# Kernel tuning notes

Measured on AMD Instinct MI355X. Metric: run time of the kernel, lower is better.

Reference implementation:

```python
import jax, jax.numpy as jnp
import numpy as np

N_NODES = 10000
N_EDGES = 320000
F = 128
N_RBF = 20


def setup_inputs() -> dict:
    key = jax.random.key(0)
    ks = jax.random.split(key, 12)
    inp = {
        "idx_i": jax.random.randint(ks[0], (N_EDGES,), 0, N_NODES),
        "idx_j": jax.random.randint(ks[1], (N_EDGES,), 0, N_NODES),
        "rel_dir": jax.random.normal(ks[2], (N_EDGES, 3), dtype=jnp.float32),
        "rel_dist_cut": jax.random.uniform(ks[3], (N_EDGES,), dtype=jnp.float32),
        "rbf_features": jax.random.normal(ks[4], (N_EDGES, N_RBF), dtype=jnp.float32),
        "scalar_features": jax.random.normal(ks[5], (N_NODES, F), dtype=jnp.float32),
        "vector_features": jax.random.normal(ks[6], (N_NODES, F, 3), dtype=jnp.float32),
        # learned params: scalar_network = Linear(F,F) -> SiLU -> Linear(F,3F); rbf_network = Linear(N_RBF,3F)
        "W1": jax.random.normal(ks[7], (F, F), dtype=jnp.float32) / np.sqrt(F),
        "b1": jnp.zeros((F,), dtype=jnp.float32),
        "W2": jax.random.normal(ks[8], (F, 3 * F), dtype=jnp.float32) / np.sqrt(F),
        "b2": jnp.zeros((3 * F,), dtype=jnp.float32),
        "Wr": jax.random.normal(ks[9], (N_RBF, 3 * F), dtype=jnp.float32) / np.sqrt(N_RBF),
        "br": jnp.zeros((3 * F,), dtype=jnp.float32),
    }
    return inp


def reference(idx_i, idx_j, rel_dir, rel_dist_cut, rbf_features,
              scalar_features, vector_features, W1, b1, W2, b2, Wr, br):
    num_nodes, num_features = scalar_features.shape
    # per-node MLP: [N, 3F]
    phi = jax.nn.silu(scalar_features @ W1 + b1) @ W2 + b2
    # distance gate: [E, 3F]
    Wg = (rbf_features @ Wr + br) * rel_dist_cut[:, None]
    # gather neighbor phi and gate
    phi_W = phi[idx_j] * Wg                       # [E, 3F]
    phi_W_vv = phi_W[:, :num_features]            # [E, F]
    phi_W_ss = phi_W[:, num_features:2 * num_features]
    phi_W_vs = phi_W[:, 2 * num_features:]
    # per-receiver edge counts (bincount)
    counts = jax.ops.segment_sum(jnp.ones((idx_i.shape[0],), phi_W.dtype),
                                 idx_i, num_segments=num_nodes)  # [N]
    scalar_residuals = jax.ops.segment_sum(phi_W_ss, idx_i, num_segments=num_nodes)
    scalar_residuals = scalar_residuals / counts[:, None]
    # per-edge vector message: [E, F, 3]
    v_edge = (vector_features[idx_j] * phi_W_vv[:, :, None]
              + phi_W_vs[:, :, None] * rel_dir[:, None, :])
    vector_residuals = jax.ops.segment_sum(v_edge, idx_i, num_segments=num_nodes)
    vector_residuals = vector_residuals / counts[:, None, None]
    return (scalar_features + scalar_residuals,
            vector_features + vector_residuals)
```

## Files before the change

kernel.cpp:

```cpp
#include <hip/hip_runtime.h>
#include <hip/hip_bf16.h>

#define NN 10000
#define NE 320000
#define FDIM 128
#define NRBF 20
#define PHI_DIM 384
#define NKEY NN
#define SCAN_BLOCKS 40

typedef unsigned int uint;
typedef unsigned short ushort;

#if __has_builtin(__builtin_amdgcn_fdot2_f32_bf16)
#define USE_DOT2 1
typedef __bf16 bf16x2 __attribute__((ext_vector_type(2)));
#else
#define USE_DOT2 0
#endif

__device__ __forceinline__ ushort f2bf(float x) {
  __hip_bfloat16 b = __float2bfloat16(x);
  return *(ushort*)&b;
}
__device__ __forceinline__ float bflo(uint u) { return __uint_as_float(u << 16); }
__device__ __forceinline__ float bfhi(uint u) { return __uint_as_float(u & 0xffff0000u); }


__global__ __launch_bounds__(256) void phi_kernel(
    const float* __restrict__ S, const float* __restrict__ W1, const float* __restrict__ b1,
    const float* __restrict__ W2, const float* __restrict__ b2, const float* __restrict__ vf,
    const int* __restrict__ idx_i, int* __restrict__ counts, char* __restrict__ tab) {
  __shared__ float s_s[8][FDIM];
  __shared__ float h_s[8][FDIM];
  const int t = threadIdx.x;
  const int tf = t & 127;
  const int half = t >> 7;
  const int nb = blockIdx.x * 8 + half * 4;
  const int row0 = half * 4;
  atomicAdd(&counts[idx_i[blockIdx.x * 256 + t]], 1);
#pragma unroll
  for (int n = 0; n < 4; n++) s_s[row0 + n][tf] = S[(nb + n) * FDIM + tf];
  __syncthreads();
  float acc[4];
#pragma unroll
  for (int n = 0; n < 4; n++) acc[n] = 0.f;
  for (int k = 0; k < FDIM; k++) {
    float w = W1[k * FDIM + tf];
#pragma unroll
    for (int n = 0; n < 4; n++) acc[n] += s_s[row0 + n][k] * w;
  }
  float bb = b1[tf];
#pragma unroll
  for (int n = 0; n < 4; n++) {
    float x = acc[n] + bb;
    h_s[row0 + n][tf] = x / (1.0f + expf(-x));
  }
  __syncthreads();
  float a0[4], a1[4], a2[4];
#pragma unroll
  for (int n = 0; n < 4; n++) { a0[n] = 0.f; a1[n] = 0.f; a2[n] = 0.f; }
  for (int k = 0; k < FDIM; k++) {
    float w0 = W2[k * PHI_DIM + tf];
    float w1 = W2[k * PHI_DIM + tf + 128];
    float w2 = W2[k * PHI_DIM + tf + 256];
#pragma unroll
    for (int n = 0; n < 4; n++) {
      float hv = h_s[row0 + n][k];
      a0[n] += hv * w0;
      a1[n] += hv * w1;
      a2[n] += hv * w2;
    }
  }
  float c0 = b2[tf], c1 = b2[tf + 128], c2 = b2[tf + 256];
#pragma unroll
  for (int n = 0; n < 4; n++) {
    const int node = nb + n;
    const float p0 = a0[n] + c0;
    const float p1 = a1[n] + c1;
    const float p2 = a2[n] + c2;
    const float* src = vf + (size_t)node * (FDIM * 3) + tf * 3;
    const uint wx = f2bf(src[0] * p0);
    const uint wy = f2bf(src[1] * p0);
    const uint wz = f2bf(src[2] * p0);
    char* pb = tab + (size_t)node * 1280;
    ((uint*)pb)[tf] = (wy << 16) | wx;
    ((uint*)(pb + 512))[tf] = ((uint)f2bf(p1) << 16) | wz;
    ((ushort*)(pb + 1024))[tf] = f2bf(p2);
  }
}

__global__ void scan1_kernel(const int* __restrict__ counts, int* __restrict__ offsets,
                             int* __restrict__ blocksums) {
  __shared__ int s[256];
  const int t = threadIdx.x;
  const int idx = blockIdx.x * 256 + t;
  const int c = counts[idx];
  s[t] = c;
  __syncthreads();
  for (int off = 1; off < 256; off <<= 1) {
    int v = (t >= off) ? s[t - off] : 0;
    __syncthreads();
    s[t] += v;
    __syncthreads();
  }
  if (idx < NKEY) offsets[idx] = s[t] - c;
  if (t == 255) blocksums[blockIdx.x] = s[255];
}

__global__ void scan2_kernel(int* __restrict__ blocksums, int* __restrict__ offsets) {
  __shared__ int s[64];
  const int t = threadIdx.x;
  int v0 = (t < SCAN_BLOCKS) ? blocksums[t] : 0;
  s[t] = v0;
  __syncthreads();
  for (int off = 1; off < 64; off <<= 1) {
    int v = (t >= off) ? s[t - off] : 0;
    __syncthreads();
    s[t] += v;
    __syncthreads();
  }
  if (t < SCAN_BLOCKS) blocksums[t] = s[t] - v0;
  if (t == SCAN_BLOCKS - 1) offsets[NKEY] = s[t];
}

__global__ void stage_kernel(const int* __restrict__ idx_i, const int* __restrict__ idx_j,
                             const float* __restrict__ cut, const float* __restrict__ dir,
                             const float* __restrict__ rbf, const int* __restrict__ offsets,
                             const int* __restrict__ blocksums, int* __restrict__ counts,
                             uint* __restrict__ edata, int* __restrict__ jlist) {
  int e = blockIdx.x * blockDim.x + threadIdx.x;
  if (e >= NE) return;
  int i = idx_i[e];
  int pos = atomicSub(&counts[i], 1) - 1;
  const int slot = offsets[i] + blocksums[i >> 8] + pos;
  jlist[slot] = idx_j[e];
  const float c = cut[e];
  uint w[12];
  w[0] = ((uint)f2bf(dir[e * 3 + 1]) << 16) | f2bf(dir[e * 3 + 0]);
  const float* rb = rbf + (size_t)e * NRBF;
#pragma unroll
  for (int r = 0; r < 10; r++) {
    uint lo = (uint)f2bf(rb[2 * r] * c);
    uint hi = (uint)f2bf(rb[2 * r + 1] * c);
    w[1 + r] = (hi << 16) | lo;
  }
  w[11] = ((uint)f2bf(dir[e * 3 + 2]) << 16) | f2bf(c);
  uint4* d = (uint4*)(edata + (size_t)slot * 12);
  d[0] = make_uint4(w[0], w[1], w[2], w[3]);
  d[1] = make_uint4(w[4], w[5], w[6], w[7]);
  d[2] = make_uint4(w[8], w[9], w[10], w[11]);
}

__global__ __launch_bounds__(128, 5) void node_kernel(
    const uint* __restrict__ edata, const int* __restrict__ jlist,
    const float* __restrict__ Wr, const float* __restrict__ br,
    const char* __restrict__ tab, const float* __restrict__ sf,
    const float* __restrict__ vf, const int* __restrict__ offsets,
    const int* __restrict__ blocksums, float* __restrict__ out) {
  const int f = threadIdx.x;
#if USE_DOT2
  bf16x2 wrA[11], wrB[11], wrC[11];
#pragma unroll
  for (int r = 0; r < 10; r++) {
    uint a = ((uint)f2bf(Wr[(2 * r + 1) * PHI_DIM + f]) << 16) | f2bf(Wr[(2 * r) * PHI_DIM + f]);
    uint b = ((uint)f2bf(Wr[(2 * r + 1) * PHI_DIM + f + 128]) << 16) |
             f2bf(Wr[(2 * r) * PHI_DIM + f + 128]);
    uint c = ((uint)f2bf(Wr[(2 * r + 1) * PHI_DIM + f + 256]) << 16) |
             f2bf(Wr[(2 * r) * PHI_DIM + f + 256]);
    wrA[r] = __builtin_bit_cast(bf16x2, a);
    wrB[r] = __builtin_bit_cast(bf16x2, b);
    wrC[r] = __builtin_bit_cast(bf16x2, c);
  }
  wrA[10] = __builtin_bit_cast(bf16x2, (uint)f2bf(br[f]));
  wrB[10] = __builtin_bit_cast(bf16x2, (uint)f2bf(br[f + 128]));
  wrC[10] = __builtin_bit_cast(bf16x2, (uint)f2bf(br[f + 256]));
#else
  float wrA[22], wrB[22], wrC[22];
#pragma unroll
  for (int r = 0; r < NRBF; r++) {
    wrA[r] = Wr[r * PHI_DIM + f];
    wrB[r] = Wr[r * PHI_DIM + f + 128];
    wrC[r] = Wr[r * PHI_DIM + f + 256];
  }
  wrA[20] = br[f];       wrA[21] = 0.f;
  wrB[20] = br[f + 128]; wrB[21] = 0.f;
  wrC[20] = br[f + 256]; wrC[21] = 0.f;
#endif
  const int n = blockIdx.x;
  const int beg = __builtin_amdgcn_readfirstlane(offsets[n] + blocksums[n >> 8]);
  const int end = __builtin_amdgcn_readfirstlane(
      (n + 1 < NKEY) ? (offsets[n + 1] + blocksums[(n + 1) >> 8]) : offsets[NKEY]);
  float ss = 0.f, ax = 0.f, ay = 0.f, az = 0.f;
  const int f4 = f * 4;

  auto process = [&](uint4 e0, uint4 e1, uint4 e2, uint d0, uint d1, uint zu) {
    uint rbp[11] = {e0.y, e0.z, e0.w, e1.x, e1.y, e1.z, e1.w, e2.x, e2.y, e2.z, e2.w};
    const float dx = bflo(e0.x);
    const float dy = bfhi(e0.x);
    const float dz = bfhi(rbp[10]);
    float g0 = 0.f, g1 = 0.f, g2 = 0.f;
#if USE_DOT2
#pragma unroll
    for (int r = 0; r < 11; r++) {
      bf16x2 rp = __builtin_bit_cast(bf16x2, rbp[r]);
      g0 = __builtin_amdgcn_fdot2_f32_bf16(rp, wrA[r], g0, false);
      g1 = __builtin_amdgcn_fdot2_f32_bf16(rp, wrB[r], g1, false);
      g2 = __builtin_amdgcn_fdot2_f32_bf16(rp, wrC[r], g2, false);
    }
#else
#pragma unroll
    for (int r = 0; r < 11; r++) {
      float rlo = bflo(rbp[r]);
      float rhi = bfhi(rbp[r]);
      g0 += rlo * wrA[2 * r] + rhi * wrA[2 * r + 1];
      g1 += rlo * wrB[2 * r] + rhi * wrB[2 * r + 1];
      g2 += rlo * wrC[2 * r] + rhi * wrC[2 * r + 1];
    }
#endif
    const float vs = bflo(zu) * g2;
    ss += bfhi(d1) * g1;
    ax += bflo(d0) * g0 + vs * dx;
    ay += bfhi(d0) * g0 + vs * dy;
    az += bflo(d1) * g0 + vs * dz;
  };

  int p = beg;
  for (; p + 2 <= end; p += 2) {
    const int j0 = __builtin_amdgcn_readfirstlane(jlist[p]);
    const int j1 = __builtin_amdgcn_readfirstlane(jlist[p + 1]);
    const char* B0 = tab + (size_t)j0 * 1280;
    const char* B1 = tab + (size_t)j1 * 1280;
    const uint d00 = *(const uint*)(B0 + f4), d01 = *(const uint*)(B0 + 512 + f4);
    const uint z0 = *(const ushort*)(B0 + 1024 + f * 2);
    const uint d10 = *(const uint*)(B1 + f4), d11 = *(const uint*)(B1 + 512 + f4);
    const uint z1 = *(const ushort*)(B1 + 1024 + f * 2);
    const uint4* r0 = (const uint4*)(edata + (size_t)p * 12);
    const uint4* r1 = (const uint4*)(edata + (size_t)(p + 1) * 12);
    uint4 a0 = r0[0], a1 = r0[1], a2 = r0[2];
    uint4 b0 = r1[0], b1 = r1[1], b2 = r1[2];
    process(a0, a1, a2, d00, d01, z0);
    process(b0, b1, b2, d10, d11, z1);
  }
  if (p < end) {
    const int j0 = __builtin_amdgcn_readfirstlane(jlist[p]);
    const char* B0 = tab + (size_t)j0 * 1280;
    const uint d00 = *(const uint*)(B0 + f4), d01 = *(const uint*)(B0 + 512 + f4);
    const uint z0 = *(const ushort*)(B0 + 1024 + f * 2);
    const uint4* r0 = (const uint4*)(edata + (size_t)p * 12);
    process(r0[0], r0[1], r0[2], d00, d01, z0);
  }

  const float inv = 1.0f / (float)(end - beg);
  out[(size_t)n * FDIM + f] = sf[(size_t)n * FDIM + f] + ss * inv;
  float* ov = out + (size_t)NN * FDIM + (size_t)n * (FDIM * 3) + f * 3;
  const float* iv = vf + (size_t)n * (FDIM * 3) + f * 3;
  ov[0] = iv[0] + ax * inv;
  ov[1] = iv[1] + ay * inv;
  ov[2] = iv[2] + az * inv;
}

extern "C" void kernel_launch(void* const* d_in, const int* in_sizes, int n_in,
                              void* d_out, int out_size, void* d_ws, size_t ws_size,
                              hipStream_t stream) {
  const int* idx_i = (const int*)d_in[0];
  const int* idx_j = (const int*)d_in[1];
  const float* rel_dir = (const float*)d_in[2];
  const float* cut = (const float*)d_in[3];
  const float* rbf = (const float*)d_in[4];
  const float* sf = (const float*)d_in[5];
  const float* vf = (const float*)d_in[6];
  const float* W1 = (const float*)d_in[7];
  const float* b1 = (const float*)d_in[8];
  const float* W2 = (const float*)d_in[9];
  const float* b2 = (const float*)d_in[10];
  const float* Wr = (const float*)d_in[11];
  const float* br = (const float*)d_in[12];
  float* out = (float*)d_out;

  char* w = (char*)d_ws;
  int* counts = (int*)w;
  int* offsets = (int*)(w + 40960);
  int* blocksums = (int*)(w + 81920);
  uint* edata = (uint*)(w + 90112);
  char* tab = w + 15450112;
  int* jlist = (int*)(w + 28250112);

  hipMemsetAsync(w, 0, 40960, stream);
  hipLaunchKernelGGL(phi_kernel, dim3(NN / 8), dim3(256), 0, stream, sf, W1, b1, W2, b2, vf,
                     idx_i, counts, tab);
  hipLaunchKernelGGL(scan1_kernel, dim3(SCAN_BLOCKS), dim3(256), 0, stream, counts, offsets,
                     blocksums);
  hipLaunchKernelGGL(scan2_kernel, dim3(1), dim3(64), 0, stream, blocksums, offsets);
  hipLaunchKernelGGL(stage_kernel, dim3((NE + 255) / 256), dim3(256), 0, stream, idx_i, idx_j,
                     cut, rel_dir, rbf, offsets, blocksums, counts, edata, jlist);
  hipLaunchKernelGGL(node_kernel, dim3(NN), dim3(128), 0, stream, edata, jlist, Wr, br, tab, sf,
                     vf, offsets, blocksums, out);
}
```

Baseline: 162.8 us.

## Compute per-edge RBF gate with MFMA in 16-edge chunks via LDS

Replaces the per-thread dot2 computation of the 384-wide distance gate with a 16x16x32 bf16 MFMA over chunks of 16 edges per node, staging the resulting gate values in LDS as bf16. The edge record is padded to 64 bytes and reordered so the RBF, bias slot and direction fields form a clean 32-wide K fragment, and the workspace offsets shift to match. This moves the small matmul from VALU dot products onto matrix cores. In exchange it adds two block barriers per chunk, wasted MFMA work for nodes with fewer than 16 edges, more edge-data traffic from the padding, an extra bf16 rounding of the gate, and a lower occupancy hint.

```diff
diff --git a/kernel.cpp b/kernel.cpp
--- a/kernel.cpp
+++ b/kernel.cpp
@@ -11,13 +11,8 @@
 
 typedef unsigned int uint;
 typedef unsigned short ushort;
-
-#if __has_builtin(__builtin_amdgcn_fdot2_f32_bf16)
-#define USE_DOT2 1
-typedef __bf16 bf16x2 __attribute__((ext_vector_type(2)));
-#else
-#define USE_DOT2 0
-#endif
+typedef __bf16 bf16x8 __attribute__((ext_vector_type(8)));
+typedef float f32x4 __attribute__((ext_vector_type(4)));
 
 __device__ __forceinline__ ushort f2bf(float x) {
   __hip_bfloat16 b = __float2bfloat16(x);
@@ -137,118 +132,132 @@
   jlist[slot] = idx_j[e];
   const float c = cut[e];
   uint w[12];
-  w[0] = ((uint)f2bf(dir[e * 3 + 1]) << 16) | f2bf(dir[e * 3 + 0]);
   const float* rb = rbf + (size_t)e * NRBF;
 #pragma unroll
   for (int r = 0; r < 10; r++) {
     uint lo = (uint)f2bf(rb[2 * r] * c);
     uint hi = (uint)f2bf(rb[2 * r + 1] * c);
-    w[1 + r] = (hi << 16) | lo;
-  }
-  w[11] = ((uint)f2bf(dir[e * 3 + 2]) << 16) | f2bf(c);
-  uint4* d = (uint4*)(edata + (size_t)slot * 12);
+    w[r] = (hi << 16) | lo;
+  }
+  w[10] = ((uint)f2bf(dir[e * 3 + 0]) << 16) | f2bf(c);
+  w[11] = ((uint)f2bf(dir[e * 3 + 2]) << 16) | f2bf(dir[e * 3 + 1]);
+  uint4* d = (uint4*)(edata + (size_t)slot * 16);
   d[0] = make_uint4(w[0], w[1], w[2], w[3]);
   d[1] = make_uint4(w[4], w[5], w[6], w[7]);
   d[2] = make_uint4(w[8], w[9], w[10], w[11]);
-}
-
-__global__ __launch_bounds__(128, 5) void node_kernel(
+  d[3] = make_uint4(0u, 0u, 0u, 0u);
+}
+
+__global__ __launch_bounds__(128, 4) void node_kernel(
     const uint* __restrict__ edata, const int* __restrict__ jlist,
     const float* __restrict__ Wr, const float* __restrict__ br,
     const char* __restrict__ tab, const float* __restrict__ sf,
     const float* __restrict__ vf, const int* __restrict__ offsets,
     const int* __restrict__ blocksums, float* __restrict__ out) {
+  __shared__ ushort wg_lds[PHI_DIM * 18];
   const int f = threadIdx.x;
-#if USE_DOT2
-  bf16x2 wrA[11], wrB[11], wrC[11];
-#pragma unroll
-  for (int r = 0; r < 10; r++) {
-    uint a = ((uint)f2bf(Wr[(2 * r + 1) * PHI_DIM + f]) << 16) | f2bf(Wr[(2 * r) * PHI_DIM + f]);
-    uint b = ((uint)f2bf(Wr[(2 * r + 1) * PHI_DIM + f + 128]) << 16) |
-             f2bf(Wr[(2 * r) * PHI_DIM + f + 128]);
-    uint c = ((uint)f2bf(Wr[(2 * r + 1) * PHI_DIM + f + 256]) << 16) |
-             f2bf(Wr[(2 * r) * PHI_DIM + f + 256]);
-    wrA[r] = __builtin_bit_cast(bf16x2, a);
-    wrB[r] = __builtin_bit_cast(bf16x2, b);
-    wrC[r] = __builtin_bit_cast(bf16x2, c);
-  }
-  wrA[10] = __builtin_bit_cast(bf16x2, (uint)f2bf(br[f]));
-  wrB[10] = __builtin_bit_cast(bf16x2, (uint)f2bf(br[f + 128]));
-  wrC[10] = __builtin_bit_cast(bf16x2, (uint)f2bf(br[f + 256]));
-#else
-  float wrA[22], wrB[22], wrC[22];
-#pragma unroll
-  for (int r = 0; r < NRBF; r++) {
-    wrA[r] = Wr[r * PHI_DIM + f];
-    wrB[r] = Wr[r * PHI_DIM + f + 128];
-    wrC[r] = Wr[r * PHI_DIM + f + 256];
-  }
-  wrA[20] = br[f];       wrA[21] = 0.f;
-  wrB[20] = br[f + 128]; wrB[21] = 0.f;
-  wrC[20] = br[f + 256]; wrC[21] = 0.f;
-#endif
+  const int lane = threadIdx.x & 63;
+  const int wv = threadIdx.x >> 6;
+  const int col = lane & 15;
+  const int kb = (lane >> 4) * 8;
+
+  bf16x8 bfrag[12];
+#pragma unroll
+  for (int t = 0; t < 12; t++) {
+    const int n = wv * 192 + t * 16 + col;
+    uint words[4];
+#pragma unroll
+    for (int p = 0; p < 4; p++) {
+      const int k0 = kb + 2 * p, k1 = k0 + 1;
+      const float v0 = (k0 < 20) ? Wr[k0 * PHI_DIM + n] : ((k0 == 20) ? br[n] : 0.f);
+      const float v1 = (k1 < 20) ? Wr[k1 * PHI_DIM + n] : ((k1 == 20) ? br[n] : 0.f);
+      words[p] = ((uint)f2bf(v1) << 16) | f2bf(v0);
+    }
+    bfrag[t] = __builtin_bit_cast(bf16x8, make_uint4(words[0], words[1], words[2], words[3]));
+  }
+
   const int n = blockIdx.x;
   const int beg = __builtin_amdgcn_readfirstlane(offsets[n] + blocksums[n >> 8]);
   const int end = __builtin_amdgcn_readfirstlane(
       (n + 1 < NKEY) ? (offsets[n + 1] + blocksums[(n + 1) >> 8]) : offsets[NKEY]);
   float ss = 0.f, ax = 0.f, ay = 0.f, az = 0.f;
   const int f4 = f * 4;
-
-  auto process = [&](uint4 e0, uint4 e1, uint4 e2, uint d0, uint d1, uint zu) {
-    uint rbp[11] = {e0.y, e0.z, e0.w, e1.x, e1.y, e1.z, e1.w, e2.x, e2.y, e2.z, e2.w};
-    const float dx = bflo(e0.x);
-    const float dy = bfhi(e0.x);
-    const float dz = bfhi(rbp[10]);
-    float g0 = 0.f, g1 = 0.f, g2 = 0.f;
-#if USE_DOT2
-#pragma unroll
-    for (int r = 0; r < 11; r++) {
-      bf16x2 rp = __builtin_bit_cast(bf16x2, rbp[r]);
-      g0 = __builtin_amdgcn_fdot2_f32_bf16(rp, wrA[r], g0, false);
-      g1 = __builtin_amdgcn_fdot2_f32_bf16(rp, wrB[r], g1, false);
-      g2 = __builtin_amdgcn_fdot2_f32_bf16(rp, wrC[r], g2, false);
-    }
-#else
-#pragma unroll
-    for (int r = 0; r < 11; r++) {
-      float rlo = bflo(rbp[r]);
-      float rhi = bfhi(rbp[r]);
-      g0 += rlo * wrA[2 * r] + rhi * wrA[2 * r + 1];
-      g1 += rlo * wrB[2 * r] + rhi * wrB[2 * r + 1];
-      g2 += rlo * wrC[2 * r] + rhi * wrC[2 * r + 1];
-    }
-#endif
-    const float vs = bflo(zu) * g2;
-    ss += bfhi(d1) * g1;
-    ax += bflo(d0) * g0 + vs * dx;
-    ay += bfhi(d0) * g0 + vs * dy;
-    az += bflo(d1) * g0 + vs * dz;
-  };
-
-  int p = beg;
-  for (; p + 2 <= end; p += 2) {
-    const int j0 = __builtin_amdgcn_readfirstlane(jlist[p]);
-    const int j1 = __builtin_amdgcn_readfirstlane(jlist[p + 1]);
-    const char* B0 = tab + (size_t)j0 * 1280;
-    const char* B1 = tab + (size_t)j1 * 1280;
-    const uint d00 = *(const uint*)(B0 + f4), d01 = *(const uint*)(B0 + 512 + f4);
-    const uint z0 = *(const ushort*)(B0 + 1024 + f * 2);
-    const uint d10 = *(const uint*)(B1 + f4), d11 = *(const uint*)(B1 + 512 + f4);
-    const uint z1 = *(const ushort*)(B1 + 1024 + f * 2);
-    const uint4* r0 = (const uint4*)(edata + (size_t)p * 12);
-    const uint4* r1 = (const uint4*)(edata + (size_t)(p + 1) * 12);
-    uint4 a0 = r0[0], a1 = r0[1], a2 = r0[2];
-    uint4 b0 = r1[0], b1 = r1[1], b2 = r1[2];
-    process(a0, a1, a2, d00, d01, z0);
-    process(b0, b1, b2, d10, d11, z1);
-  }
-  if (p < end) {
-    const int j0 = __builtin_amdgcn_readfirstlane(jlist[p]);
-    const char* B0 = tab + (size_t)j0 * 1280;
-    const uint d00 = *(const uint*)(B0 + f4), d01 = *(const uint*)(B0 + 512 + f4);
-    const uint z0 = *(const ushort*)(B0 + 1024 + f * 2);
-    const uint4* r0 = (const uint4*)(edata + (size_t)p * 12);
-    process(r0[0], r0[1], r0[2], d00, d01, z0);
+  const char* ebytes = (const char*)edata;
+
+  for (int chunk = beg; chunk < end; chunk += 16) {
+    const int m = min(16, end - chunk);
+    bf16x8 afrag = __builtin_bit_cast(bf16x8, make_uint4(0u, 0u, 0u, 0u));
+    if (col < m)
+      afrag = __builtin_bit_cast(
+          bf16x8, *(const uint4*)(ebytes + (size_t)(chunk + col) * 64 + (size_t)(lane >> 4) * 16));
+#pragma unroll
+    for (int t = 0; t < 12; t++) {
+      f32x4 acc = {0.f, 0.f, 0.f, 0.f};
+      acc = __builtin_amdgcn_mfma_f32_16x16x32_bf16(afrag, bfrag[t], acc, 0, 0, 0);
+      const int nc = wv * 192 + t * 16 + col;
+      const int r0 = (lane >> 4) * 4;
+      uint lo = ((uint)f2bf(acc[1]) << 16) | f2bf(acc[0]);
+      uint hi = ((uint)f2bf(acc[3]) << 16) | f2bf(acc[2]);
+      uint* dst = (uint*)&wg_lds[nc * 18 + r0];
+      dst[0] = lo;
+      dst[1] = hi;
+    }
+    __syncthreads();
+    int q = 0;
+    for (; q + 2 <= m; q += 2) {
+      const uint gu0 = *(const uint*)&wg_lds[f * 18 + q];
+      const uint gu1 = *(const uint*)&wg_lds[(f + 128) * 18 + q];
+      const uint gu2 = *(const uint*)&wg_lds[(f + 256) * 18 + q];
+      const int j0 = __builtin_amdgcn_readfirstlane(jlist[chunk + q]);
+      const int j1 = __builtin_amdgcn_readfirstlane(jlist[chunk + q + 1]);
+      const uint* er0 = edata + (size_t)(chunk + q) * 16;
+      const uint* er1 = edata + (size_t)(chunk + q + 1) * 16;
+      const uint cdx0 = __builtin_amdgcn_readfirstlane(er0[10]);
+      const uint dyz0 = __builtin_amdgcn_readfirstlane(er0[11]);
+      const uint cdx1 = __builtin_amdgcn_readfirstlane(er1[10]);
+      const uint dyz1 = __builtin_amdgcn_readfirstlane(er1[11]);
+      const char* B0 = tab + (size_t)j0 * 1280;
+      const char* B1 = tab + (size_t)j1 * 1280;
+      const uint d00 = *(const uint*)(B0 + f4), d01 = *(const uint*)(B0 + 512 + f4);
+      const uint z0u = *(const ushort*)(B0 + 1024 + f * 2);
+      const uint d10 = *(const uint*)(B1 + f4), d11 = *(const uint*)(B1 + 512 + f4);
+      const uint z1u = *(const ushort*)(B1 + 1024 + f * 2);
+      {
+        const float g0 = bflo(gu0), g1 = bflo(gu1), g2 = bflo(gu2);
+        const float vs = bflo(z0u) * g2;
+        ss += bfhi(d01) * g1;
+        ax += bflo(d00) * g0 + vs * bfhi(cdx0);
+        ay += bfhi(d00) * g0 + vs * bflo(dyz0);
+        az += bflo(d01) * g0 + vs * bfhi(dyz0);
+      }
+      {
+        const float g0 = bfhi(gu0), g1 = bfhi(gu1), g2 = bfhi(gu2);
+        const float vs = bflo(z1u) * g2;
+        ss += bfhi(d11) * g1;
+        ax += bflo(d10) * g0 + vs * bfhi(cdx1);
+        ay += bfhi(d10) * g0 + vs * bflo(dyz1);
+        az += bflo(d11) * g0 + vs * bfhi(dyz1);
+      }
+    }
+    if (q < m) {
+      const uint gu0 = wg_lds[f * 18 + q];
+      const uint gu1 = wg_lds[(f + 128) * 18 + q];
+      const uint gu2 = wg_lds[(f + 256) * 18 + q];
+      const int j0 = __builtin_amdgcn_readfirstlane(jlist[chunk + q]);
+      const uint* er0 = edata + (size_t)(chunk + q) * 16;
+      const uint cdx0 = __builtin_amdgcn_readfirstlane(er0[10]);
+      const uint dyz0 = __builtin_amdgcn_readfirstlane(er0[11]);
+      const char* B0 = tab + (size_t)j0 * 1280;
+      const uint d00 = *(const uint*)(B0 + f4), d01 = *(const uint*)(B0 + 512 + f4);
+      const uint z0u = *(const ushort*)(B0 + 1024 + f * 2);
+      const float g0 = bflo(gu0), g1 = bflo(gu1), g2 = bflo(gu2);
+      const float vs = bflo(z0u) * g2;
+      ss += bfhi(d01) * g1;
+      ax += bflo(d00) * g0 + vs * bfhi(cdx0);
+      ay += bfhi(d00) * g0 + vs * bflo(dyz0);
+      az += bflo(d01) * g0 + vs * bfhi(dyz0);
+    }
+    __syncthreads();
   }
 
   const float inv = 1.0f / (float)(end - beg);
@@ -283,8 +292,8 @@
   int* offsets = (int*)(w + 40960);
   int* blocksums = (int*)(w + 81920);
   uint* edata = (uint*)(w + 90112);
-  char* tab = w + 15450112;
-  int* jlist = (int*)(w + 28250112);
+  char* tab = w + 20570112;
+  int* jlist = (int*)(w + 33370112);
 
   hipMemsetAsync(w, 0, 40960, stream);
   hipLaunchKernelGGL(phi_kernel, dim3(NN / 8), dim3(256), 0, stream, sf, W1, b1, W2, b2, vf,
```

Result: slower. 235.0 us (+44.3%).

## Sort edges by sender bucket and process five receivers per block in bucket order

Applied to the files above, without the earlier changes.

Edges are now keyed by (sender bucket, receiver), so the counting sort groups each receiver's edges by which sixteenth of the node range their sender falls in. The node kernel handles five receivers per block and walks the buckets in order, so concurrently running blocks gather phi/vector table rows from a narrower address window and get better cache locality. In exchange there are 16x more sort keys, a larger scan and memset, more register pressure from five accumulator sets (occupancy hint lowered from 5 to 4), and fewer, longer blocks.

```diff
diff --git a/kernel.cpp b/kernel.cpp
--- a/kernel.cpp
+++ b/kernel.cpp
@@ -6,8 +6,9 @@
 #define FDIM 128
 #define NRBF 20
 #define PHI_DIM 384
-#define NKEY NN
-#define SCAN_BLOCKS 40
+#define NBUCK 16
+#define NKEY (NN * NBUCK)
+#define SCAN_BLOCKS 626
 
 typedef unsigned int uint;
 typedef unsigned short ushort;
@@ -25,12 +26,14 @@
 }
 __device__ __forceinline__ float bflo(uint u) { return __uint_as_float(u << 16); }
 __device__ __forceinline__ float bfhi(uint u) { return __uint_as_float(u & 0xffff0000u); }
+__device__ __forceinline__ int jbucket(int j) { return (int)(((uint)j * NBUCK) / NN); }
 
 
 __global__ __launch_bounds__(256) void phi_kernel(
     const float* __restrict__ S, const float* __restrict__ W1, const float* __restrict__ b1,
     const float* __restrict__ W2, const float* __restrict__ b2, const float* __restrict__ vf,
-    const int* __restrict__ idx_i, int* __restrict__ counts, char* __restrict__ tab) {
+    const int* __restrict__ idx_i, const int* __restrict__ idx_j, int* __restrict__ counts,
+    char* __restrict__ tab) {
   __shared__ float s_s[8][FDIM];
   __shared__ float h_s[8][FDIM];
   const int t = threadIdx.x;
@@ -38,7 +41,10 @@
   const int half = t >> 7;
   const int nb = blockIdx.x * 8 + half * 4;
   const int row0 = half * 4;
-  atomicAdd(&counts[idx_i[blockIdx.x * 256 + t]], 1);
+  {
+    const int e = blockIdx.x * 256 + t;
+    atomicAdd(&counts[jbucket(idx_j[e]) * NN + idx_i[e]], 1);
+  }
 #pragma unroll
   for (int n = 0; n < 4; n++) s_s[row0 + n][tf] = S[(nb + n) * FDIM + tf];
   __syncthreads();
@@ -109,19 +115,19 @@
 }
 
 __global__ void scan2_kernel(int* __restrict__ blocksums, int* __restrict__ offsets) {
-  __shared__ int s[64];
+  __shared__ int s[1024];
   const int t = threadIdx.x;
   int v0 = (t < SCAN_BLOCKS) ? blocksums[t] : 0;
   s[t] = v0;
   __syncthreads();
-  for (int off = 1; off < 64; off <<= 1) {
+  for (int off = 1; off < 1024; off <<= 1) {
     int v = (t >= off) ? s[t - off] : 0;
     __syncthreads();
     s[t] += v;
     __syncthreads();
   }
   if (t < SCAN_BLOCKS) blocksums[t] = s[t] - v0;
-  if (t == SCAN_BLOCKS - 1) offsets[NKEY] = s[t];
+  if (t == 1023) offsets[NKEY] = s[t];
 }
 
 __global__ void stage_kernel(const int* __restrict__ idx_i, const int* __restrict__ idx_j,
@@ -131,10 +137,11 @@
                              uint* __restrict__ edata, int* __restrict__ jlist) {
   int e = blockIdx.x * blockDim.x + threadIdx.x;
   if (e >= NE) return;
-  int i = idx_i[e];
-  int pos = atomicSub(&counts[i], 1) - 1;
-  const int slot = offsets[i] + blocksums[i >> 8] + pos;
-  jlist[slot] = idx_j[e];
+  const int j = idx_j[e];
+  const int key = jbucket(j) * NN + idx_i[e];
+  int pos = atomicSub(&counts[key], 1) - 1;
+  const int slot = offsets[key] + blocksums[key >> 8] + pos;
+  jlist[slot] = j;
   const float c = cut[e];
   uint w[12];
   w[0] = ((uint)f2bf(dir[e * 3 + 1]) << 16) | f2bf(dir[e * 3 + 0]);
@@ -152,7 +159,7 @@
   d[2] = make_uint4(w[8], w[9], w[10], w[11]);
 }
 
-__global__ __launch_bounds__(128, 5) void node_kernel(
+__global__ __launch_bounds__(128, 4) void node_kernel(
     const uint* __restrict__ edata, const int* __restrict__ jlist,
     const float* __restrict__ Wr, const float* __restrict__ br,
     const char* __restrict__ tab, const float* __restrict__ sf,
@@ -187,77 +194,109 @@
   wrB[20] = br[f + 128]; wrB[21] = 0.f;
   wrC[20] = br[f + 256]; wrC[21] = 0.f;
 #endif
-  const int n = blockIdx.x;
-  const int beg = __builtin_amdgcn_readfirstlane(offsets[n] + blocksums[n >> 8]);
-  const int end = __builtin_amdgcn_readfirstlane(
-      (n + 1 < NKEY) ? (offsets[n + 1] + blocksums[(n + 1) >> 8]) : offsets[NKEY]);
-  float ss = 0.f, ax = 0.f, ay = 0.f, az = 0.f;
+  const int n0 = blockIdx.x * 5;
   const int f4 = f * 4;
-
-  auto process = [&](uint4 e0, uint4 e1, uint4 e2, uint d0, uint d1, uint zu) {
-    uint rbp[11] = {e0.y, e0.z, e0.w, e1.x, e1.y, e1.z, e1.w, e2.x, e2.y, e2.z, e2.w};
-    const float dx = bflo(e0.x);
-    const float dy = bfhi(e0.x);
-    const float dz = bfhi(rbp[10]);
-    float g0 = 0.f, g1 = 0.f, g2 = 0.f;
+  float ss0 = 0, ax0 = 0, ay0 = 0, az0 = 0;
+  float ss1 = 0, ax1 = 0, ay1 = 0, az1 = 0;
+  float ss2 = 0, ax2 = 0, ay2 = 0, az2 = 0;
+  float ss3 = 0, ax3 = 0, ay3 = 0, az3 = 0;
+  float ss4 = 0, ax4 = 0, ay4 = 0, az4 = 0;
+  int c0n = 0, c1n = 0, c2n = 0, c3n = 0, c4n = 0;
+
+  auto runSeg = [&](int segBeg, int segEnd, float& ss, float& ax, float& ay, float& az) {
+    auto process = [&](uint4 e0, uint4 e1, uint4 e2, uint d0, uint d1, uint zu) {
+      uint rbp[11] = {e0.y, e0.z, e0.w, e1.x, e1.y, e1.z, e1.w, e2.x, e2.y, e2.z, e2.w};
+      const float dx = bflo(e0.x);
+      const float dy = bfhi(e0.x);
+      const float dz = bfhi(rbp[10]);
+      float g0 = 0.f, g1 = 0.f, g2 = 0.f;
 #if USE_DOT2
 #pragma unroll
-    for (int r = 0; r < 11; r++) {
-      bf16x2 rp = __builtin_bit_cast(bf16x2, rbp[r]);
-      g0 = __builtin_amdgcn_fdot2_f32_bf16(rp, wrA[r], g0, false);
-      g1 = __builtin_amdgcn_fdot2_f32_bf16(rp, wrB[r], g1, false);
-      g2 = __builtin_amdgcn_fdot2_f32_bf16(rp, wrC[r], g2, false);
+      for (int r = 0; r < 11; r++) {
+        bf16x2 rp = __builtin_bit_cast(bf16x2, rbp[r]);
+        g0 = __builtin_amdgcn_fdot2_f32_bf16(rp, wrA[r], g0, false);
+        g1 = __builtin_amdgcn_fdot2_f32_bf16(rp, wrB[r], g1, false);
+        g2 = __builtin_amdgcn_fdot2_f32_bf16(rp, wrC[r], g2, false);
+      }
+#else
+#pragma unroll
+      for (int r = 0; r < 11; r++) {
+        float rlo = bflo(rbp[r]);
+        float rhi = bfhi(rbp[r]);
+        g0 += rlo * wrA[2 * r] + rhi * wrA[2 * r + 1];
+        g1 += rlo * wrB[2 * r] + rhi * wrB[2 * r + 1];
+        g2 += rlo * wrC[2 * r] + rhi * wrC[2 * r + 1];
+      }
+#endif
+      const float vs = bflo(zu) * g2;
+      ss += bfhi(d1) * g1;
+      ax += bflo(d0) * g0 + vs * dx;
+      ay += bfhi(d0) * g0 + vs * dy;
+      az += bflo(d1) * g0 + vs * dz;
+    };
+    int p = segBeg;
+    for (; p + 2 <= segEnd; p += 2) {
+      const int j0 = __builtin_amdgcn_readfirstlane(jlist[p]);
+      const int j1 = __builtin_amdgcn_readfirstlane(jlist[p + 1]);
+      const char* B0 = tab + (size_t)j0 * 1280;
+      const char* B1 = tab + (size_t)j1 * 1280;
+      const uint d00 = *(const uint*)(B0 + f4), d01 = *(const uint*)(B0 + 512 + f4);
+      const uint z0 = *(const ushort*)(B0 + 1024 + f * 2);
+      const uint d10 = *(const uint*)(B1 + f4), d11 = *(const uint*)(B1 + 512 + f4);
+      const uint z1 = *(const ushort*)(B1 + 1024 + f * 2);
+      const uint4* r0 = (const uint4*)(edata + (size_t)p * 12);
+      const uint4* r1 = (const uint4*)(edata + (size_t)(p + 1) * 12);
+      uint4 a0 = r0[0], a1 = r0[1], a2 = r0[2];
+      uint4 b0 = r1[0], b1 = r1[1], b2 = r1[2];
+      process(a0, a1, a2, d00, d01, z0);
+      process(b0, b1, b2, d10, d11, z1);
     }
-#else
-#pragma unroll
-    for (int r = 0; r < 11; r++) {
-      float rlo = bflo(rbp[r]);
-      float rhi = bfhi(rbp[r]);
-      g0 += rlo * wrA[2 * r] + rhi * wrA[2 * r + 1];
-      g1 += rlo * wrB[2 * r] + rhi * wrB[2 * r + 1];
-      g2 += rlo * wrC[2 * r] + rhi * wrC[2 * r + 1];
+    if (p < segEnd) {
+      const int j0 = __builtin_amdgcn_readfirstlane(jlist[p]);
+      const char* B0 = tab + (size_t)j0 * 1280;
+      const uint d00 = *(const uint*)(B0 + f4), d01 = *(const uint*)(B0 + 512 + f4);
+      const uint z0 = *(const ushort*)(B0 + 1024 + f * 2);
+      const uint4* r0 = (const uint4*)(edata + (size_t)p * 12);
+      process(r0[0], r0[1], r0[2], d00, d01, z0);
     }
-#endif
-    const float vs = bflo(zu) * g2;
-    ss += bfhi(d1) * g1;
-    ax += bflo(d0) * g0 + vs * dx;
-    ay += bfhi(d0) * g0 + vs * dy;
-    az += bflo(d1) * g0 + vs * dz;
   };
 
-  int p = beg;
-  for (; p + 2 <= end; p += 2) {
-    const int j0 = __builtin_amdgcn_readfirstlane(jlist[p]);
-    const int j1 = __builtin_amdgcn_readfirstlane(jlist[p + 1]);
-    const char* B0 = tab + (size_t)j0 * 1280;
-    const char* B1 = tab + (size_t)j1 * 1280;
-    const uint d00 = *(const uint*)(B0 + f4), d01 = *(const uint*)(B0 + 512 + f4);
-    const uint z0 = *(const ushort*)(B0 + 1024 + f * 2);
-    const uint d10 = *(const uint*)(B1 + f4), d11 = *(const uint*)(B1 + 512 + f4);
-    const uint z1 = *(const ushort*)(B1 + 1024 + f * 2);
-    const uint4* r0 = (const uint4*)(edata + (size_t)p * 12);
-    const uint4* r1 = (const uint4*)(edata + (size_t)(p + 1) * 12);
-    uint4 a0 = r0[0], a1 = r0[1], a2 = r0[2];
-    uint4 b0 = r1[0], b1 = r1[1], b2 = r1[2];
-    process(a0, a1, a2, d00, d01, z0);
-    process(b0, b1, b2, d10, d11, z1);
-  }
-  if (p < end) {
-    const int j0 = __builtin_amdgcn_readfirstlane(jlist[p]);
-    const char* B0 = tab + (size_t)j0 * 1280;
-    const uint d00 = *(const uint*)(B0 + f4), d01 = *(const uint*)(B0 + 512 + f4);
-    const uint z0 = *(const ushort*)(B0 + 1024 + f * 2);
-    const uint4* r0 = (const uint4*)(edata + (size_t)p * 12);
-    process(r0[0], r0[1], r0[2], d00, d01, z0);
-  }
-
-  const float inv = 1.0f / (float)(end - beg);
-  out[(size_t)n * FDIM + f] = sf[(size_t)n * FDIM + f] + ss * inv;
-  float* ov = out + (size_t)NN * FDIM + (size_t)n * (FDIM * 3) + f * 3;
-  const float* iv = vf + (size_t)n * (FDIM * 3) + f * 3;
-  ov[0] = iv[0] + ax * inv;
-  ov[1] = iv[1] + ay * inv;
-  ov[2] = iv[2] + az * inv;
+  for (int b = 0; b < NBUCK; b++) {
+    const int base = b * NN + n0;
+    int o[6];
+#pragma unroll
+    for (int q = 0; q < 6; q++) {
+      const int key = base + q;
+      o[q] = __builtin_amdgcn_readfirstlane(
+          (key < NKEY) ? (offsets[key] + blocksums[key >> 8]) : offsets[NKEY]);
+    }
+    runSeg(o[0], o[1], ss0, ax0, ay0, az0);
+    runSeg(o[1], o[2], ss1, ax1, ay1, az1);
+    runSeg(o[2], o[3], ss2, ax2, ay2, az2);
+    runSeg(o[3], o[4], ss3, ax3, ay3, az3);
+    runSeg(o[4], o[5], ss4, ax4, ay4, az4);
+    c0n += o[1] - o[0];
+    c1n += o[2] - o[1];
+    c2n += o[3] - o[2];
+    c3n += o[4] - o[3];
+    c4n += o[5] - o[4];
+  }
+
+  auto writeOut = [&](int s, int cnt, float ss, float ax, float ay, float az) {
+    const int i = n0 + s;
+    const float inv = 1.0f / (float)cnt;
+    out[(size_t)i * FDIM + f] = sf[(size_t)i * FDIM + f] + ss * inv;
+    float* ov = out + (size_t)NN * FDIM + (size_t)i * (FDIM * 3) + f * 3;
+    const float* iv = vf + (size_t)i * (FDIM * 3) + f * 3;
+    ov[0] = iv[0] + ax * inv;
+    ov[1] = iv[1] + ay * inv;
+    ov[2] = iv[2] + az * inv;
+  };
+  writeOut(0, c0n, ss0, ax0, ay0, az0);
+  writeOut(1, c1n, ss1, ax1, ay1, az1);
+  writeOut(2, c2n, ss2, ax2, ay2, az2);
+  writeOut(3, c3n, ss3, ax3, ay3, az3);
+  writeOut(4, c4n, ss4, ax4, ay4, az4);
 }
 
 extern "C" void kernel_launch(void* const* d_in, const int* in_sizes, int n_in,
@@ -280,20 +319,20 @@
 
   char* w = (char*)d_ws;
   int* counts = (int*)w;
-  int* offsets = (int*)(w + 40960);
-  int* blocksums = (int*)(w + 81920);
-  uint* edata = (uint*)(w + 90112);
-  char* tab = w + 15450112;
-  int* jlist = (int*)(w + 28250112);
-
-  hipMemsetAsync(w, 0, 40960, stream);
+  int* offsets = (int*)(w + 641024);
+  int* blocksums = (int*)(w + 1281088);
+  uint* edata = (uint*)(w + 1283648);
+  char* tab = w + 16643648;
+  int* jlist = (int*)(w + 29443648);
+
+  hipMemsetAsync(w, 0, 641024, stream);
   hipLaunchKernelGGL(phi_kernel, dim3(NN / 8), dim3(256), 0, stream, sf, W1, b1, W2, b2, vf,
-                     idx_i, counts, tab);
+                     idx_i, idx_j, counts, tab);
   hipLaunchKernelGGL(scan1_kernel, dim3(SCAN_BLOCKS), dim3(256), 0, stream, counts, offsets,
                      blocksums);
-  hipLaunchKernelGGL(scan2_kernel, dim3(1), dim3(64), 0, stream, blocksums, offsets);
+  hipLaunchKernelGGL(scan2_kernel, dim3(1), dim3(1024), 0, stream, blocksums, offsets);
   hipLaunchKernelGGL(stage_kernel, dim3((NE + 255) / 256), dim3(256), 0, stream, idx_i, idx_j,
                      cut, rel_dir, rbf, offsets, blocksums, counts, edata, jlist);
-  hipLaunchKernelGGL(node_kernel, dim3(NN), dim3(128), 0, stream, edata, jlist, Wr, br, tab, sf,
-                     vf, offsets, blocksums, out);
-}
+  hipLaunchKernelGGL(node_kernel, dim3(NN / 5), dim3(128), 0, stream, edata, jlist, Wr, br, tab,
+                     sf, vf, offsets, blocksums, out);
+}
```

Result: slower. 178.7 us (median of 2 runs) (+9.7%).

## Bucket edges by neighbor index range within each receiver to improve gather locality

Applied to the files above, without the earlier changes.

Edges are now counting-sorted by a composite key of (neighbor-index bucket, receiver), using four buckets over idx_j. Each node block walks its edges bucket by bucket, so the many concurrent blocks tend to gather phi/vector rows from the same quarter of the node table at once. The aim is to shrink the working set of the random gathers so more of them hit in L2. In exchange the count/scan arrays grow fourfold, with a larger memset, more scan blocks and a wider second-level scan, and the node kernel gains an extra loop with four offset lookups per node.

```diff
diff --git a/kernel.cpp b/kernel.cpp
--- a/kernel.cpp
+++ b/kernel.cpp
@@ -6,8 +6,9 @@
 #define FDIM 128
 #define NRBF 20
 #define PHI_DIM 384
-#define NKEY NN
-#define SCAN_BLOCKS 40
+#define NBUCK 4
+#define NKEY (NN * NBUCK)
+#define SCAN_BLOCKS 157
 
 typedef unsigned int uint;
 typedef unsigned short ushort;
@@ -25,12 +26,14 @@
 }
 __device__ __forceinline__ float bflo(uint u) { return __uint_as_float(u << 16); }
 __device__ __forceinline__ float bfhi(uint u) { return __uint_as_float(u & 0xffff0000u); }
+__device__ __forceinline__ int jbucket(int j) { return (int)(((uint)j * NBUCK) / NN); }
 
 
 __global__ __launch_bounds__(256) void phi_kernel(
     const float* __restrict__ S, const float* __restrict__ W1, const float* __restrict__ b1,
     const float* __restrict__ W2, const float* __restrict__ b2, const float* __restrict__ vf,
-    const int* __restrict__ idx_i, int* __restrict__ counts, char* __restrict__ tab) {
+    const int* __restrict__ idx_i, const int* __restrict__ idx_j, int* __restrict__ counts,
+    char* __restrict__ tab) {
   __shared__ float s_s[8][FDIM];
   __shared__ float h_s[8][FDIM];
   const int t = threadIdx.x;
@@ -38,7 +41,10 @@
   const int half = t >> 7;
   const int nb = blockIdx.x * 8 + half * 4;
   const int row0 = half * 4;
-  atomicAdd(&counts[idx_i[blockIdx.x * 256 + t]], 1);
+  {
+    const int e = blockIdx.x * 256 + t;
+    atomicAdd(&counts[jbucket(idx_j[e]) * NN + idx_i[e]], 1);
+  }
 #pragma unroll
   for (int n = 0; n < 4; n++) s_s[row0 + n][tf] = S[(nb + n) * FDIM + tf];
   __syncthreads();
@@ -109,19 +115,19 @@
 }
 
 __global__ void scan2_kernel(int* __restrict__ blocksums, int* __restrict__ offsets) {
-  __shared__ int s[64];
+  __shared__ int s[256];
   const int t = threadIdx.x;
   int v0 = (t < SCAN_BLOCKS) ? blocksums[t] : 0;
   s[t] = v0;
   __syncthreads();
-  for (int off = 1; off < 64; off <<= 1) {
+  for (int off = 1; off < 256; off <<= 1) {
     int v = (t >= off) ? s[t - off] : 0;
     __syncthreads();
     s[t] += v;
     __syncthreads();
   }
   if (t < SCAN_BLOCKS) blocksums[t] = s[t] - v0;
-  if (t == SCAN_BLOCKS - 1) offsets[NKEY] = s[t];
+  if (t == 255) offsets[NKEY] = s[t];
 }
 
 __global__ void stage_kernel(const int* __restrict__ idx_i, const int* __restrict__ idx_j,
@@ -131,10 +137,11 @@
                              uint* __restrict__ edata, int* __restrict__ jlist) {
   int e = blockIdx.x * blockDim.x + threadIdx.x;
   if (e >= NE) return;
-  int i = idx_i[e];
-  int pos = atomicSub(&counts[i], 1) - 1;
-  const int slot = offsets[i] + blocksums[i >> 8] + pos;
-  jlist[slot] = idx_j[e];
+  const int j = idx_j[e];
+  const int key = jbucket(j) * NN + idx_i[e];
+  int pos = atomicSub(&counts[key], 1) - 1;
+  const int slot = offsets[key] + blocksums[key >> 8] + pos;
+  jlist[slot] = j;
   const float c = cut[e];
   uint w[12];
   w[0] = ((uint)f2bf(dir[e * 3 + 1]) << 16) | f2bf(dir[e * 3 + 0]);
@@ -188,11 +195,9 @@
   wrC[20] = br[f + 256]; wrC[21] = 0.f;
 #endif
   const int n = blockIdx.x;
-  const int beg = __builtin_amdgcn_readfirstlane(offsets[n] + blocksums[n >> 8]);
-  const int end = __builtin_amdgcn_readfirstlane(
-      (n + 1 < NKEY) ? (offsets[n + 1] + blocksums[(n + 1) >> 8]) : offsets[NKEY]);
+  const int f4 = f * 4;
   float ss = 0.f, ax = 0.f, ay = 0.f, az = 0.f;
-  const int f4 = f * 4;
+  int cnt = 0;
 
   auto process = [&](uint4 e0, uint4 e1, uint4 e2, uint d0, uint d1, uint zu) {
     uint rbp[11] = {e0.y, e0.z, e0.w, e1.x, e1.y, e1.z, e1.w, e2.x, e2.y, e2.z, e2.w};
@@ -225,33 +230,41 @@
     az += bflo(d1) * g0 + vs * dz;
   };
 
-  int p = beg;
-  for (; p + 2 <= end; p += 2) {
-    const int j0 = __builtin_amdgcn_readfirstlane(jlist[p]);
-    const int j1 = __builtin_amdgcn_readfirstlane(jlist[p + 1]);
-    const char* B0 = tab + (size_t)j0 * 1280;
-    const char* B1 = tab + (size_t)j1 * 1280;
-    const uint d00 = *(const uint*)(B0 + f4), d01 = *(const uint*)(B0 + 512 + f4);
-    const uint z0 = *(const ushort*)(B0 + 1024 + f * 2);
-    const uint d10 = *(const uint*)(B1 + f4), d11 = *(const uint*)(B1 + 512 + f4);
-    const uint z1 = *(const ushort*)(B1 + 1024 + f * 2);
-    const uint4* r0 = (const uint4*)(edata + (size_t)p * 12);
-    const uint4* r1 = (const uint4*)(edata + (size_t)(p + 1) * 12);
-    uint4 a0 = r0[0], a1 = r0[1], a2 = r0[2];
-    uint4 b0 = r1[0], b1 = r1[1], b2 = r1[2];
-    process(a0, a1, a2, d00, d01, z0);
-    process(b0, b1, b2, d10, d11, z1);
-  }
-  if (p < end) {
-    const int j0 = __builtin_amdgcn_readfirstlane(jlist[p]);
-    const char* B0 = tab + (size_t)j0 * 1280;
-    const uint d00 = *(const uint*)(B0 + f4), d01 = *(const uint*)(B0 + 512 + f4);
-    const uint z0 = *(const ushort*)(B0 + 1024 + f * 2);
-    const uint4* r0 = (const uint4*)(edata + (size_t)p * 12);
-    process(r0[0], r0[1], r0[2], d00, d01, z0);
-  }
-
-  const float inv = 1.0f / (float)(end - beg);
+  for (int b = 0; b < NBUCK; b++) {
+    const int k0 = b * NN + n;
+    const int beg = __builtin_amdgcn_readfirstlane(offsets[k0] + blocksums[k0 >> 8]);
+    const int k1 = k0 + 1;
+    const int end = __builtin_amdgcn_readfirstlane(
+        (k1 < NKEY) ? (offsets[k1] + blocksums[k1 >> 8]) : offsets[NKEY]);
+    cnt += end - beg;
+    int p = beg;
+    for (; p + 2 <= end; p += 2) {
+      const int j0 = __builtin_amdgcn_readfirstlane(jlist[p]);
+      const int j1 = __builtin_amdgcn_readfirstlane(jlist[p + 1]);
+      const char* B0 = tab + (size_t)j0 * 1280;
+      const char* B1 = tab + (size_t)j1 * 1280;
+      const uint d00 = *(const uint*)(B0 + f4), d01 = *(const uint*)(B0 + 512 + f4);
+      const uint z0 = *(const ushort*)(B0 + 1024 + f * 2);
+      const uint d10 = *(const uint*)(B1 + f4), d11 = *(const uint*)(B1 + 512 + f4);
+      const uint z1 = *(const ushort*)(B1 + 1024 + f * 2);
+      const uint4* r0 = (const uint4*)(edata + (size_t)p * 12);
+      const uint4* r1 = (const uint4*)(edata + (size_t)(p + 1) * 12);
+      uint4 a0 = r0[0], a1 = r0[1], a2 = r0[2];
+      uint4 b0 = r1[0], b1 = r1[1], b2 = r1[2];
+      process(a0, a1, a2, d00, d01, z0);
+      process(b0, b1, b2, d10, d11, z1);
+    }
+    if (p < end) {
+      const int j0 = __builtin_amdgcn_readfirstlane(jlist[p]);
+      const char* B0 = tab + (size_t)j0 * 1280;
+      const uint d00 = *(const uint*)(B0 + f4), d01 = *(const uint*)(B0 + 512 + f4);
+      const uint z0 = *(const ushort*)(B0 + 1024 + f * 2);
+      const uint4* r0 = (const uint4*)(edata + (size_t)p * 12);
+      process(r0[0], r0[1], r0[2], d00, d01, z0);
+    }
+  }
+
+  const float inv = 1.0f / (float)cnt;
   out[(size_t)n * FDIM + f] = sf[(size_t)n * FDIM + f] + ss * inv;
   float* ov = out + (size_t)NN * FDIM + (size_t)n * (FDIM * 3) + f * 3;
   const float* iv = vf + (size_t)n * (FDIM * 3) + f * 3;
@@ -280,18 +293,18 @@
 
   char* w = (char*)d_ws;
   int* counts = (int*)w;
-  int* offsets = (int*)(w + 40960);
-  int* blocksums = (int*)(w + 81920);
-  uint* edata = (uint*)(w + 90112);
-  char* tab = w + 15450112;
-  int* jlist = (int*)(w + 28250112);
-
-  hipMemsetAsync(w, 0, 40960, stream);
+  int* offsets = (int*)(w + 163840);
+  int* blocksums = (int*)(w + 327680);
+  uint* edata = (uint*)(w + 328704);
+  char* tab = w + 15688704;
+  int* jlist = (int*)(w + 28488704);
+
+  hipMemsetAsync(w, 0, 163840, stream);
   hipLaunchKernelGGL(phi_kernel, dim3(NN / 8), dim3(256), 0, stream, sf, W1, b1, W2, b2, vf,
-                     idx_i, counts, tab);
+                     idx_i, idx_j, counts, tab);
   hipLaunchKernelGGL(scan1_kernel, dim3(SCAN_BLOCKS), dim3(256), 0, stream, counts, offsets,
                      blocksums);
-  hipLaunchKernelGGL(scan2_kernel, dim3(1), dim3(64), 0, stream, blocksums, offsets);
+  hipLaunchKernelGGL(scan2_kernel, dim3(1), dim3(256), 0, stream, blocksums, offsets);
   hipLaunchKernelGGL(stage_kernel, dim3((NE + 255) / 256), dim3(256), 0, stream, idx_i, idx_j,
                      cut, rel_dir, rbf, offsets, blocksums, counts, edata, jlist);
   hipLaunchKernelGGL(node_kernel, dim3(NN), dim3(128), 0, stream, edata, jlist, Wr, br, tab, sf,
```

After: 153.6 us. -5.7%, faster.
